# Kernel optimization log

Hardware: AMD Instinct MI355X
Metric: run time of the kernel (lower is better)

## Reference

```python
import jax, jax.numpy as jnp
import numpy as np

B, H, W = 64, 480, 640      # batch, cartesian iris image size
PH, PW = 64, 512            # polar grid
FS, NF = 15, 7              # BSIF filter size / count


def setup_inputs() -> dict:
    key = jax.random.key(0)
    k1, k2, k3, k4, k5, k6 = jax.random.split(key, 6)
    image = jax.random.uniform(k1, (B, 1, H, W), jnp.float32)
    pcx = jax.random.uniform(k2, (B,), jnp.float32, 280.0, 360.0)
    pcy = jax.random.uniform(k3, (B,), jnp.float32, 200.0, 280.0)
    pr = jax.random.uniform(k4, (B,), jnp.float32, 30.0, 60.0)
    ir = jax.random.uniform(k5, (B,), jnp.float32, 90.0, 130.0)
    pupil_xyr = jnp.stack([pcx, pcy, pr], axis=-1)
    iris_xyr = jnp.stack([pcx, pcy, ir], axis=-1)
    filter_mat = jax.random.normal(k6, (FS, FS, NF), jnp.float32)
    return {"image": image, "pupil_xyr": pupil_xyr, "iris_xyr": iris_xyr,
            "filter_mat": filter_mat}


def _bilinear_sample(img, gx, gy):
    """torch.nn.functional.grid_sample, mode=bilinear, align_corners=False,
    padding_mode=zeros. img [B,C,H,W]; gx,gy [B,Hg,Wg] normalized coords."""
    _, _, Hi, Wi = img.shape
    x = ((gx + 1.0) * Wi - 1.0) / 2.0
    y = ((gy + 1.0) * Hi - 1.0) / 2.0
    x0 = jnp.floor(x); y0 = jnp.floor(y)
    wx = x - x0; wy = y - y0

    def gather(ix, iy):
        valid = (ix >= 0) & (ix < Wi) & (iy >= 0) & (iy < Hi)
        ixc = jnp.clip(ix, 0, Wi - 1).astype(jnp.int32)
        iyc = jnp.clip(iy, 0, Hi - 1).astype(jnp.int32)
        v = jax.vmap(lambda im, yy, xx: im[:, yy, xx])(img, iyc, ixc)  # [B,C,Hg,Wg]
        return v * valid[:, None].astype(img.dtype)

    v00 = gather(x0, y0); v01 = gather(x0 + 1, y0)
    v10 = gather(x0, y0 + 1); v11 = gather(x0 + 1, y0 + 1)
    wx = wx[:, None]; wy = wy[:, None]  # [B,1,Hg,Wg]
    return (v00 * (1 - wx) * (1 - wy) + v01 * wx * (1 - wy)
            + v10 * (1 - wx) * wy + v11 * wx * wy)


def _forward(image, pupil_xyr, iris_xyr, filter_mat):
    image_scaled = image * 255.0
    _, _, Hc, Wc = image_scaled.shape

    # --- cartToPol: polar sampling grid from pupil/iris circles ---
    theta = 2.0 * jnp.pi * jnp.arange(1, PW + 1, dtype=jnp.float32) / PW
    cosT, sinT = jnp.cos(theta), jnp.sin(theta)                     # [PW]
    pxc = pupil_xyr[:, 0:1] + pupil_xyr[:, 2:3] * cosT[None]        # [B,PW]
    pyc = pupil_xyr[:, 1:2] + pupil_xyr[:, 2:3] * sinT[None]
    ixc = iris_xyr[:, 0:1] + iris_xyr[:, 2:3] * cosT[None]
    iyc = iris_xyr[:, 1:2] + iris_xyr[:, 2:3] * sinT[None]
    radius = jnp.linspace(0.0, 1.0, PH)[:, None]                    # [PH,1]
    xg = (1 - radius)[None] * pxc[:, None, :] + radius[None] * ixc[:, None, :]  # [B,PH,PW]
    yg = (1 - radius)[None] * pyc[:, None, :] + radius[None] * iyc[:, None, :]
    x = jnp.clip(xg, 0.0, Wc - 1.0)
    y = jnp.clip(yg, 0.0, Hc - 1.0)
    x_norm = x / (Wc - 1) * 2.0 - 1.0
    y_norm = y / (Hc - 1) * 2.0 - 1.0
    # module's custom grid_sample pre-transform (half-pixel re-normalization)
    gx = ((x_norm + 1.0) / 2.0 * Wc - 0.5) / (Wc - 1) * 2.0 - 1.0
    gy = ((y_norm + 1.0) / 2.0 * Hc - 0.5) / (Hc - 1) * 2.0 - 1.0
    image_polar = _bilinear_sample(image_scaled, gx, gy)            # [B,1,PH,PW]

    # --- getCodes: toroidal wrap pad + conv filter bank ---
    r = FS // 2
    img_wrap = jnp.pad(image_polar, ((0, 0), (0, 0), (r, r), (r, r)), mode="wrap")
    # torch: moveaxis(filter[None], 3, 0) -> (NF,1,FS,FS), then flip along dim 0
    weight = jnp.flip(jnp.transpose(filter_mat, (2, 0, 1))[:, None, :, :], axis=0)
    codes = jax.lax.conv_general_dilated(
        img_wrap, weight, window_strides=(1, 1), padding="VALID",
        dimension_numbers=("NCHW", "OIHW", "NCHW"))                 # [B,NF,PH,PW]

    # --- gram matrix ---
    a, b, c, d = codes.shape
    feats = codes.reshape(a * b, c * d)
    gram = (feats @ feats.T) / (a * b * c * d)                      # [a*b, a*b]
    return codes, gram, image_polar


def reference(image, pupil_xyr, iris_xyr, filter_mat):
    return _forward(image, pupil_xyr, iris_xyr, filter_mat)
```

## Files before the change

### kernel.cpp

```cpp
#include <hip/hip_runtime.h>
#include <math.h>

#define BB 64
#define HH 480
#define WW 640
#define PH 64
#define PW 512
#define FS 15
#define NF 7
#define RR 7
#define GD 448
#define KTOT 32768

#define GSPL 32
#define KPB (KTOT / GSPL)
#define GSTK 64
#define GNST (KPB / GSTK)
#define GPLW 66

#define FSPL 32
#define FKPB (KTOT / FSPL)
#define GBK 32
#define GNB (FKPB / GBK)
#define PLW 40

#define CJT 32
#define CSP 52
#define CSPD 26
#define CSROWS 31
#define CSY 46

static constexpr long CODES_N = (long)BB * NF * PH * PW;
static constexpr long GRAM_N  = (long)GD * GD;
static constexpr long POLAR_N = (long)BB * PH * PW;
static constexpr size_t BF_BYTES   = (size_t)GD * KTOT * 2;
static constexpr size_t PART_BYTES = (size_t)GSPL * GRAM_N * 4;
static constexpr size_t WTAB_BYTES = 512 * 16;

typedef __bf16    bf16x4   __attribute__((ext_vector_type(4)));
typedef __bf16    bf16x8   __attribute__((ext_vector_type(8)));
typedef _Float16  f16x8    __attribute__((ext_vector_type(8)));
typedef float     floatx4  __attribute__((ext_vector_type(4)));
typedef float     floatx16 __attribute__((ext_vector_type(16)));

__constant__ int c_by[28] = {0,0,0,0,0,0,0, 1,1,1,1,1,1, 2,2,2,2,2, 3,3,3,3, 4,4,4, 5,5, 6};
__constant__ int c_bx[28] = {0,1,2,3,4,5,6, 1,2,3,4,5,6, 2,3,4,5,6, 3,4,5,6, 4,5,6, 5,6, 6};

__device__ __forceinline__ float wfrag_val(const float* fm, int s, int l, int e) {
    int du = l >> 5;
    int v0 = ((l >> 4) & 1) * 8;
    int n  = l & 15;
    int jd = (n >= NF) ? 1 : 0;
    int o  = n - NF * jd;
    int u  = 2 * s + du;
    int v  = v0 + e;
    int vp = v - jd;
    float wv = 0.0f;
    if (n < 2 * NF && u < FS && vp >= 0 && vp < FS)
        wv = fm[(u * FS + vp) * NF + (NF - 1 - o)];
    return wv;
}

__global__ __launch_bounds__(256) void polar_kernel(
        const float* __restrict__ img,
        const float* __restrict__ pupil,
        const float* __restrict__ iris,
        const float* __restrict__ fm,
        float* __restrict__ polar,
        _Float16* __restrict__ wtab) {
    if (wtab && blockIdx.x == 0) {
        #pragma unroll
        for (int ss = 0; ss < 2; ++ss) {
            int slot = threadIdx.x + ss * 256;
            int s = slot >> 6, l = slot & 63;
            f16x8 vv;
            #pragma unroll
            for (int e = 0; e < 8; ++e) vv[e] = (_Float16)wfrag_val(fm, s, l, e);
            *(f16x8*)&wtab[slot * 8] = vv;
        }
    }

    int t = blockIdx.x * 256 + threadIdx.x;
    if (t >= (int)POLAR_N) return;
    int j = t & (PW - 1);
    int i = (t >> 9) & (PH - 1);
    int b = t >> 15;

    float theta = 6.2831855f * (float)(j + 1) / (float)PW;
    float s, c;
    __sincosf(theta, &s, &c);

    float pcx = pupil[b * 3 + 0], pcy = pupil[b * 3 + 1], pr = pupil[b * 3 + 2];
    float icx = iris[b * 3 + 0],  icy = iris[b * 3 + 1],  ir = iris[b * 3 + 2];

    float px = pcx + pr * c;
    float py = pcy + pr * s;
    float ix = icx + ir * c;
    float iy = icy + ir * s;

    float r = (float)i / 63.0f;
    float xg = (1.0f - r) * px + r * ix;
    float yg = (1.0f - r) * py + r * iy;

    float x = fminf(fmaxf(xg, 0.0f), (float)(WW - 1));
    float y = fminf(fmaxf(yg, 0.0f), (float)(HH - 1));

    float xn = x / (float)(WW - 1) * 2.0f - 1.0f;
    float gx = ((xn + 1.0f) / 2.0f * (float)WW - 0.5f) / (float)(WW - 1) * 2.0f - 1.0f;
    float xs = ((gx + 1.0f) * (float)WW - 1.0f) / 2.0f;

    float yn = y / (float)(HH - 1) * 2.0f - 1.0f;
    float gy = ((yn + 1.0f) / 2.0f * (float)HH - 0.5f) / (float)(HH - 1) * 2.0f - 1.0f;
    float ys = ((gy + 1.0f) * (float)HH - 1.0f) / 2.0f;

    float x0f = floorf(xs), y0f = floorf(ys);
    float wx = xs - x0f, wy = ys - y0f;
    int x0 = (int)x0f, y0 = (int)y0f;

    const float* im = img + (size_t)b * (HH * WW);
    float v00 = 0.f, v01 = 0.f, v10 = 0.f, v11 = 0.f;
    bool xv0 = (x0 >= 0) & (x0 < WW);
    bool xv1 = (x0 + 1 >= 0) & (x0 + 1 < WW);
    bool yv0 = (y0 >= 0) & (y0 < HH);
    bool yv1 = (y0 + 1 >= 0) & (y0 + 1 < HH);
    if (xv0 & yv0) v00 = im[(size_t)y0 * WW + x0];
    if (xv1 & yv0) v01 = im[(size_t)y0 * WW + x0 + 1];
    if (xv0 & yv1) v10 = im[(size_t)(y0 + 1) * WW + x0];
    if (xv1 & yv1) v11 = im[(size_t)(y0 + 1) * WW + x0 + 1];

    float val = v00 * (1.0f - wx) * (1.0f - wy) + v01 * wx * (1.0f - wy)
              + v10 * (1.0f - wx) * wy          + v11 * wx * wy;
    polar[t] = val * 255.0f;
}

__global__ __launch_bounds__(256) void conv_mfma_kernel(
        const float* __restrict__ polar,
        const float* __restrict__ fm,
        const _Float16* __restrict__ wtab,
        float* __restrict__ codes,
        __bf16* __restrict__ cbf) {
    __shared__ __align__(16) _Float16 stg[CSROWS * CSP];
    __shared__ __align__(16) float outBuf[NF * 16 * CJT];

    int bid = blockIdx.x;
    int b   = bid >> 6;
    int jt  = (bid >> 2) & 15;
    int it  = bid & 3;
    int j0  = jt * CJT;
    int i0  = it * 16;
    int tid  = threadIdx.x;
    int lane = tid & 63;
    int w    = tid >> 6;

    const float* pb = polar + (size_t)b * (PH * PW);

    for (int e = tid; e < CSROWS * CSY; e += 256) {
        int r = e / CSY;
        int y = e - r * CSY;
        int grow = (i0 + r - RR) & (PH - 1);
        int gcol = (j0 - RR + y) & (PW - 1);
        stg[r * CSP + y] = (_Float16)pb[grow * PW + gcol];
    }

    f16x8 Wreg[8];
    if (wtab) {
        #pragma unroll
        for (int s = 0; s < 8; ++s)
            Wreg[s] = *(const f16x8*)&wtab[(s * 64 + lane) * 8];
        __syncthreads();
    } else {
        uint4* Wb = (uint4*)outBuf;
        for (int slot = tid; slot < 512; slot += 256) {
            int s = slot >> 6, l = slot & 63;
            f16x8 vv;
            #pragma unroll
            for (int e2 = 0; e2 < 8; ++e2) vv[e2] = (_Float16)wfrag_val(fm, s, l, e2);
            Wb[slot] = *(const uint4*)&vv;
        }
        __syncthreads();
        #pragma unroll
        for (int s = 0; s < 8; ++s)
            Wreg[s] = *(const f16x8*)&Wb[s * 64 + lane];
        __syncthreads();
    }

    const unsigned int* stg32 = (const unsigned int*)stg;
    int mrow = lane & 15;
    int du   = lane >> 5;
    int v0h  = ((lane >> 4) & 1) * 4;
    int n    = lane & 15;
    int jd   = (n >= NF) ? 1 : 0;
    int o    = n - NF * jd;
    int g4   = lane >> 4;

    floatx4 acc0 = {}, acc1 = {}, acc2 = {}, acc3 = {};
    #pragma unroll
    for (int s = 0; s < 8; ++s) {
        int dbase = CSPD * (mrow + du + 2 * s) + 4 * w + v0h;
        uint2 u01 = *(const uint2*)&stg32[dbase + 0];
        uint2 u23 = *(const uint2*)&stg32[dbase + 2];
        uint2 u45 = *(const uint2*)&stg32[dbase + 4];
        uint2 u67 = *(const uint2*)&stg32[dbase + 6];
        unsigned int ud0 = u01.x, ud1 = u01.y, ud2 = u23.x, ud3 = u23.y;
        unsigned int ud4 = u45.x, ud5 = u45.y, ud6 = u67.x, ud7 = u67.y;
        uint4 a0 = make_uint4(ud0, ud1, ud2, ud3);
        uint4 a1 = make_uint4(ud1, ud2, ud3, ud4);
        uint4 a2 = make_uint4(ud2, ud3, ud4, ud5);
        uint4 a3 = make_uint4(ud3, ud4, ud5, ud6);
        (void)ud7;
        acc0 = __builtin_amdgcn_mfma_f32_16x16x32_f16(*(const f16x8*)&a0, Wreg[s], acc0, 0, 0, 0);
        acc1 = __builtin_amdgcn_mfma_f32_16x16x32_f16(*(const f16x8*)&a1, Wreg[s], acc1, 0, 0, 0);
        acc2 = __builtin_amdgcn_mfma_f32_16x16x32_f16(*(const f16x8*)&a2, Wreg[s], acc2, 0, 0, 0);
        acc3 = __builtin_amdgcn_mfma_f32_16x16x32_f16(*(const f16x8*)&a3, Wreg[s], acc3, 0, 0, 0);
    }
    if (n < 2 * NF) {
        #pragma unroll
        for (int r = 0; r < 4; ++r) {
            int orow = (o * 16 + (4 * g4 + r)) * CJT;
            outBuf[orow + 2 * (w * 4 + 0) + jd] = acc0[r];
            outBuf[orow + 2 * (w * 4 + 1) + jd] = acc1[r];
            outBuf[orow + 2 * (w * 4 + 2) + jd] = acc2[r];
            outBuf[orow + 2 * (w * 4 + 3) + jd] = acc3[r];
        }
    }
    __syncthreads();
    for (int g = tid; g < NF * 16 * (CJT / 4); g += 256) {
        int oo  = g >> 7;
        int rem = g & 127;
        int il  = rem >> 3;
        int j4  = rem & 7;
        float4 v = *(const float4*)&outBuf[(oo * 16 + il) * CJT + j4 * 4];
        size_t gbase = (((size_t)b * NF + oo) * PH + i0 + il) * PW + j0 + j4 * 4;
        *(float4*)&codes[gbase] = v;
        if (cbf) {
            bf16x4 bv;
            bv[0] = (__bf16)v.x; bv[1] = (__bf16)v.y;
            bv[2] = (__bf16)v.z; bv[3] = (__bf16)v.w;
            *(bf16x4*)&cbf[gbase] = bv;
        }
    }
}

__global__ __launch_bounds__(256) void gram_bf_kernel(
        const __bf16* __restrict__ feats,
        float* __restrict__ partials) {
    __shared__ __bf16 Ab[2][64][GPLW];
    __shared__ __bf16 Bb[2][64][GPLW];

    int pi = blockIdx.x;
    int by = c_by[pi], bx = c_bx[pi];
    int p0 = by * 64, q0 = bx * 64;
    size_t kbase = (size_t)blockIdx.y * KPB;

    int tid = threadIdx.x;
    int lane = tid & 63;
    int w = tid >> 6;
    int wr = w >> 1, wc = w & 1;

    int srow = tid >> 3;
    int slot = tid & 7;
    const __bf16* apA  = feats + (size_t)(p0 + srow) * KTOT + kbase + slot * 8;
    const __bf16* apA2 = apA + (size_t)32 * KTOT;
    const __bf16* apB  = feats + (size_t)(q0 + srow) * KTOT + kbase + slot * 8;
    const __bf16* apB2 = apB + (size_t)32 * KTOT;

    int arow = 32 * wr + (lane & 31);
    int brow = 32 * wc + (lane & 31);
    int ko = (lane >> 5) * 8;

    floatx16 acc = {};

    bf16x8 ra0 = *(const bf16x8*)(apA);
    bf16x8 ra1 = *(const bf16x8*)(apA2);
    bf16x8 rb0 = *(const bf16x8*)(apB);
    bf16x8 rb1 = *(const bf16x8*)(apB2);
    bf16x8 na0 = *(const bf16x8*)(apA + GSTK);
    bf16x8 na1 = *(const bf16x8*)(apA2 + GSTK);
    bf16x8 nb0 = *(const bf16x8*)(apB + GSTK);
    bf16x8 nb1 = *(const bf16x8*)(apB2 + GSTK);

    for (int s = 0; s < GNST; ++s) {
        int p = s & 1;
        *(bf16x8*)&Ab[p][srow][slot * 8]      = ra0;
        *(bf16x8*)&Ab[p][srow + 32][slot * 8] = ra1;
        *(bf16x8*)&Bb[p][srow][slot * 8]      = rb0;
        *(bf16x8*)&Bb[p][srow + 32][slot * 8] = rb1;
        __syncthreads();
        ra0 = na0; ra1 = na1; rb0 = nb0; rb1 = nb1;
        if (s + 2 < GNST) {
            size_t off = (size_t)(s + 2) * GSTK;
            na0 = *(const bf16x8*)(apA + off);
            na1 = *(const bf16x8*)(apA2 + off);
            nb0 = *(const bf16x8*)(apB + off);
            nb1 = *(const bf16x8*)(apB2 + off);
        }
        #pragma unroll
        for (int st = 0; st < 4; ++st) {
            bf16x8 af = *(const bf16x8*)&Ab[p][arow][st * 16 + ko];
            bf16x8 bg = *(const bf16x8*)&Bb[p][brow][st * 16 + ko];
            acc = __builtin_amdgcn_mfma_f32_32x32x16_bf16(af, bg, acc, 0, 0, 0);
        }
    }

    float* part = partials + (size_t)blockIdx.y * GRAM_N;
    int col = lane & 31;
    #pragma unroll
    for (int r = 0; r < 16; ++r) {
        int row = (r & 3) + 8 * (r >> 2) + 4 * (lane >> 5);
        int p = p0 + 32 * wr + row;
        int q = q0 + 32 * wc + col;
        float v = acc[r];
        part[(size_t)p * GD + q] = v;
        if (bx != by) part[(size_t)q * GD + p] = v;
    }
}

__global__ __launch_bounds__(256) void gram_reduce_kernel(
        const float* __restrict__ partials,
        float* __restrict__ gram) {
    int t = blockIdx.x * 256 + threadIdx.x;
    const float scale = 1.0f / 14680064.0f;
    float4 s = make_float4(0.f, 0.f, 0.f, 0.f);
    #pragma unroll
    for (int sp = 0; sp < GSPL; ++sp) {
        float4 v = *(const float4*)&partials[(size_t)sp * GRAM_N + (size_t)t * 4];
        s.x += v.x; s.y += v.y; s.z += v.z; s.w += v.w;
    }
    s.x *= scale; s.y *= scale; s.z *= scale; s.w *= scale;
    *(float4*)&gram[(size_t)t * 4] = s;
}

__device__ __forceinline__ void split4(float4 v, bf16x4& h, bf16x4& l) {
    float x[4] = {v.x, v.y, v.z, v.w};
    #pragma unroll
    for (int j = 0; j < 4; ++j) {
        __bf16 hh = (__bf16)x[j];
        h[j] = hh;
        l[j] = (__bf16)(x[j] - (float)hh);
    }
}

__global__ __launch_bounds__(256) void gram_hilo_kernel(
        const float* __restrict__ feats,
        float* __restrict__ gram) {
    __shared__ __bf16 Ah[2][64][PLW], Al[2][64][PLW];
    __shared__ __bf16 Bh[2][64][PLW], Bl[2][64][PLW];

    int pi = blockIdx.x;
    int by = c_by[pi], bx = c_bx[pi];
    int p0 = by * 64, q0 = bx * 64;
    int kbase = blockIdx.y * FKPB;

    int tid = threadIdx.x;
    int lane = tid & 63;
    int w = tid >> 6;
    int wr = w >> 1, wc = w & 1;

    int r0 = tid >> 3;
    int slot = tid & 7;
    const float* ap0 = feats + (size_t)(p0 + r0)      * KTOT + kbase + slot * 4;
    const float* ap1 = feats + (size_t)(p0 + r0 + 32) * KTOT + kbase + slot * 4;
    const float* bp0 = feats + (size_t)(q0 + r0)      * KTOT + kbase + slot * 4;
    const float* bp1 = feats + (size_t)(q0 + r0 + 32) * KTOT + kbase + slot * 4;

    int frow = lane & 31;
    int arow = 32 * wr + frow;
    int brow = 32 * wc + frow;
    int kq = (lane >> 5) * 8;

    floatx16 acc = {};

    {
        float4 a0 = *(const float4*)ap0;
        float4 a1 = *(const float4*)ap1;
        float4 b0 = *(const float4*)bp0;
        float4 b1 = *(const float4*)bp1;
        bf16x4 h, l;
        split4(a0, h, l); *(bf16x4*)&Ah[0][r0][slot*4] = h;      *(bf16x4*)&Al[0][r0][slot*4] = l;
        split4(a1, h, l); *(bf16x4*)&Ah[0][r0+32][slot*4] = h;   *(bf16x4*)&Al[0][r0+32][slot*4] = l;
        split4(b0, h, l); *(bf16x4*)&Bh[0][r0][slot*4] = h;      *(bf16x4*)&Bl[0][r0][slot*4] = l;
        split4(b1, h, l); *(bf16x4*)&Bh[0][r0+32][slot*4] = h;   *(bf16x4*)&Bl[0][r0+32][slot*4] = l;
    }
    __syncthreads();

    for (int s = 0; s < GNB; ++s) {
        int buf = s & 1;
        float4 a0, a1, b0, b1;
        if (s + 1 < GNB) {
            int off = (s + 1) * GBK;
            a0 = *(const float4*)(ap0 + off);
            a1 = *(const float4*)(ap1 + off);
            b0 = *(const float4*)(bp0 + off);
            b1 = *(const float4*)(bp1 + off);
        }
        #pragma unroll
        for (int kk = 0; kk < 2; ++kk) {
            int ko = kq + kk * 16;
            bf16x8 ah = *(const bf16x8*)&Ah[buf][arow][ko];
            bf16x8 al = *(const bf16x8*)&Al[buf][arow][ko];
            bf16x8 bh = *(const bf16x8*)&Bh[buf][brow][ko];
            bf16x8 bl = *(const bf16x8*)&Bl[buf][brow][ko];
            acc = __builtin_amdgcn_mfma_f32_32x32x16_bf16(ah, bh, acc, 0, 0, 0);
            acc = __builtin_amdgcn_mfma_f32_32x32x16_bf16(ah, bl, acc, 0, 0, 0);
            acc = __builtin_amdgcn_mfma_f32_32x32x16_bf16(al, bh, acc, 0, 0, 0);
        }
        if (s + 1 < GNB) {
            int nb = (s + 1) & 1;
            bf16x4 h, l;
            split4(a0, h, l); *(bf16x4*)&Ah[nb][r0][slot*4] = h;      *(bf16x4*)&Al[nb][r0][slot*4] = l;
            split4(a1, h, l); *(bf16x4*)&Ah[nb][r0+32][slot*4] = h;   *(bf16x4*)&Al[nb][r0+32][slot*4] = l;
            split4(b0, h, l); *(bf16x4*)&Bh[nb][r0][slot*4] = h;      *(bf16x4*)&Bl[nb][r0][slot*4] = l;
            split4(b1, h, l); *(bf16x4*)&Bh[nb][r0+32][slot*4] = h;   *(bf16x4*)&Bl[nb][r0+32][slot*4] = l;
        }
        __syncthreads();
    }

    const float scale = 1.0f / 14680064.0f;
    int col = lane & 31;
    #pragma unroll
    for (int r = 0; r < 16; ++r) {
        int row = (r & 3) + 8 * (r >> 2) + 4 * (lane >> 5);
        int p = p0 + 32 * wr + row;
        int q = q0 + 32 * wc + col;
        float v = acc[r] * scale;
        atomicAdd(&gram[(size_t)p * GD + q], v);
        if (bx != by) atomicAdd(&gram[(size_t)q * GD + p], v);
    }
}

extern "C" void kernel_launch(void* const* d_in, const int* in_sizes, int n_in,
                              void* d_out, int out_size, void* d_ws, size_t ws_size,
                              hipStream_t stream) {
    const float* img   = (const float*)d_in[0];
    const float* pupil = (const float*)d_in[1];
    const float* iris  = (const float*)d_in[2];
    const float* fm    = (const float*)d_in[3];

    float* codes = (float*)d_out;
    float* gram  = codes + CODES_N;
    float* polar = gram + GRAM_N;

    bool use_bf = (ws_size >= BF_BYTES + PART_BYTES + WTAB_BYTES);
    __bf16* cbf = use_bf ? (__bf16*)d_ws : nullptr;
    float* partials = (float*)((char*)d_ws + BF_BYTES);
    _Float16* wtab = use_bf ? (_Float16*)((char*)d_ws + BF_BYTES + PART_BYTES) : nullptr;

    polar_kernel<<<(int)(POLAR_N / 256), 256, 0, stream>>>(img, pupil, iris, fm, polar, wtab);

    conv_mfma_kernel<<<BB * 16 * 4, 256, 0, stream>>>(polar, fm, wtab, codes, cbf);

    if (use_bf) {
        dim3 ggrid(28, GSPL);
        gram_bf_kernel<<<ggrid, 256, 0, stream>>>((const __bf16*)d_ws, partials);
        gram_reduce_kernel<<<(int)(GRAM_N / 4 / 256), 256, 0, stream>>>(partials, gram);
    } else {
        hipMemsetAsync(gram, 0, GRAM_N * sizeof(float), stream);
        dim3 ggrid(28, FSPL);
        gram_hilo_kernel<<<ggrid, 256, 0, stream>>>(codes, gram);
    }
}
```

Before: 206.7 us.

## Pad shared-memory tiles to cut bank conflicts and halve gram K-split

Halves the number of K-splits in the gram kernel, which doubles the work per block and halves the partial buffers the reduce kernel has to sum. Widens the gram LDS row pitch to 68 and splits the 16-byte LDS accesses into 8-byte halves so they stay aligned with the new pitch. Reorders and pads the conv output staging buffer (pitch 36, row-major by output row then filter) to reduce LDS bank conflicts. The trade-offs are fewer gram blocks in flight and twice as many LDS instructions per access.

```diff
diff --git a/kernel.cpp b/kernel.cpp
--- a/kernel.cpp
+++ b/kernel.cpp
@@ -12,11 +12,11 @@
 #define GD 448
 #define KTOT 32768
 
-#define GSPL 32
+#define GSPL 16
 #define KPB (KTOT / GSPL)
 #define GSTK 64
 #define GNST (KPB / GSTK)
-#define GPLW 66
+#define GPLW 68
 
 #define FSPL 32
 #define FKPB (KTOT / FSPL)
@@ -29,6 +29,7 @@
 #define CSPD 26
 #define CSROWS 31
 #define CSY 46
+#define OBP 36
 
 static constexpr long CODES_N = (long)BB * NF * PH * PW;
 static constexpr long GRAM_N  = (long)GD * GD;
@@ -42,6 +43,8 @@
 typedef _Float16  f16x8    __attribute__((ext_vector_type(8)));
 typedef float     floatx4  __attribute__((ext_vector_type(4)));
 typedef float     floatx16 __attribute__((ext_vector_type(16)));
+
+union bfu { bf16x8 v; bf16x4 h[2]; };
 
 __constant__ int c_by[28] = {0,0,0,0,0,0,0, 1,1,1,1,1,1, 2,2,2,2,2, 3,3,3,3, 4,4,4, 5,5, 6};
 __constant__ int c_bx[28] = {0,1,2,3,4,5,6, 1,2,3,4,5,6, 2,3,4,5,6, 3,4,5,6, 4,5,6, 5,6, 6};
@@ -140,7 +143,7 @@
         float* __restrict__ codes,
         __bf16* __restrict__ cbf) {
     __shared__ __align__(16) _Float16 stg[CSROWS * CSP];
-    __shared__ __align__(16) float outBuf[NF * 16 * CJT];
+    __shared__ __align__(16) float outBuf[16 * NF * OBP];
 
     int bid = blockIdx.x;
     int b   = bid >> 6;
@@ -216,7 +219,8 @@
     if (n < 2 * NF) {
         #pragma unroll
         for (int r = 0; r < 4; ++r) {
-            int orow = (o * 16 + (4 * g4 + r)) * CJT;
+            int il = 4 * g4 + r;
+            int orow = (il * NF + o) * OBP;
             outBuf[orow + 2 * (w * 4 + 0) + jd] = acc0[r];
             outBuf[orow + 2 * (w * 4 + 1) + jd] = acc1[r];
             outBuf[orow + 2 * (w * 4 + 2) + jd] = acc2[r];
@@ -229,7 +233,7 @@
         int rem = g & 127;
         int il  = rem >> 3;
         int j4  = rem & 7;
-        float4 v = *(const float4*)&outBuf[(oo * 16 + il) * CJT + j4 * 4];
+        float4 v = *(const float4*)&outBuf[(il * NF + oo) * OBP + j4 * 4];
         size_t gbase = (((size_t)b * NF + oo) * PH + i0 + il) * PW + j0 + j4 * 4;
         *(float4*)&codes[gbase] = v;
         if (cbf) {
@@ -270,35 +274,43 @@
 
     floatx16 acc = {};
 
-    bf16x8 ra0 = *(const bf16x8*)(apA);
-    bf16x8 ra1 = *(const bf16x8*)(apA2);
-    bf16x8 rb0 = *(const bf16x8*)(apB);
-    bf16x8 rb1 = *(const bf16x8*)(apB2);
-    bf16x8 na0 = *(const bf16x8*)(apA + GSTK);
-    bf16x8 na1 = *(const bf16x8*)(apA2 + GSTK);
-    bf16x8 nb0 = *(const bf16x8*)(apB + GSTK);
-    bf16x8 nb1 = *(const bf16x8*)(apB2 + GSTK);
+    bfu ra0, ra1, rb0, rb1, na0, na1, nb0, nb1;
+    ra0.v = *(const bf16x8*)(apA);
+    ra1.v = *(const bf16x8*)(apA2);
+    rb0.v = *(const bf16x8*)(apB);
+    rb1.v = *(const bf16x8*)(apB2);
+    na0.v = *(const bf16x8*)(apA + GSTK);
+    na1.v = *(const bf16x8*)(apA2 + GSTK);
+    nb0.v = *(const bf16x8*)(apB + GSTK);
+    nb1.v = *(const bf16x8*)(apB2 + GSTK);
 
     for (int s = 0; s < GNST; ++s) {
         int p = s & 1;
-        *(bf16x8*)&Ab[p][srow][slot * 8]      = ra0;
-        *(bf16x8*)&Ab[p][srow + 32][slot * 8] = ra1;
-        *(bf16x8*)&Bb[p][srow][slot * 8]      = rb0;
-        *(bf16x8*)&Bb[p][srow + 32][slot * 8] = rb1;
+        *(bf16x4*)&Ab[p][srow][slot * 8]          = ra0.h[0];
+        *(bf16x4*)&Ab[p][srow][slot * 8 + 4]      = ra0.h[1];
+        *(bf16x4*)&Ab[p][srow + 32][slot * 8]     = ra1.h[0];
+        *(bf16x4*)&Ab[p][srow + 32][slot * 8 + 4] = ra1.h[1];
+        *(bf16x4*)&Bb[p][srow][slot * 8]          = rb0.h[0];
+        *(bf16x4*)&Bb[p][srow][slot * 8 + 4]      = rb0.h[1];
+        *(bf16x4*)&Bb[p][srow + 32][slot * 8]     = rb1.h[0];
+        *(bf16x4*)&Bb[p][srow + 32][slot * 8 + 4] = rb1.h[1];
         __syncthreads();
         ra0 = na0; ra1 = na1; rb0 = nb0; rb1 = nb1;
         if (s + 2 < GNST) {
             size_t off = (size_t)(s + 2) * GSTK;
-            na0 = *(const bf16x8*)(apA + off);
-            na1 = *(const bf16x8*)(apA2 + off);
-            nb0 = *(const bf16x8*)(apB + off);
-            nb1 = *(const bf16x8*)(apB2 + off);
+            na0.v = *(const bf16x8*)(apA + off);
+            na1.v = *(const bf16x8*)(apA2 + off);
+            nb0.v = *(const bf16x8*)(apB + off);
+            nb1.v = *(const bf16x8*)(apB2 + off);
         }
         #pragma unroll
         for (int st = 0; st < 4; ++st) {
-            bf16x8 af = *(const bf16x8*)&Ab[p][arow][st * 16 + ko];
-            bf16x8 bg = *(const bf16x8*)&Bb[p][brow][st * 16 + ko];
-            acc = __builtin_amdgcn_mfma_f32_32x32x16_bf16(af, bg, acc, 0, 0, 0);
+            bfu af, bg;
+            af.h[0] = *(const bf16x4*)&Ab[p][arow][st * 16 + ko];
+            af.h[1] = *(const bf16x4*)&Ab[p][arow][st * 16 + ko + 4];
+            bg.h[0] = *(const bf16x4*)&Bb[p][brow][st * 16 + ko];
+            bg.h[1] = *(const bf16x4*)&Bb[p][brow][st * 16 + ko + 4];
+            acc = __builtin_amdgcn_mfma_f32_32x32x16_bf16(af.v, bg.v, acc, 0, 0, 0);
         }
     }
 
```

New measurement: 194.6 us. 5.9% less time.
